# Optimization experiments

Measured on AMD Instinct MI355X. Metric: run time of the kernel, lower is better.

## Reference

```python
import jax, jax.numpy as jnp
import numpy as np

N = 2048          # num nodes
C = 256           # dense_dim per input
EMB = 3 * C       # 768
H = 8             # num_heads
D = EMB // H      # 96 head_dim
ALPHA = 0.2       # leaky relu slope
SCALE = D ** -0.5


def setup_inputs() -> dict:
    key = jax.random.key(0)
    ks = jax.random.split(key, 9)
    sd = EMB ** -0.5
    return {
        "eh": jax.random.normal(ks[0], (N, C), jnp.float32),
        "er": jax.random.normal(ks[1], (N, C), jnp.float32),
        "et": jax.random.normal(ks[2], (N, C), jnp.float32),
        "h_id": jax.random.randint(ks[3], (N,), 0, 32),
        "W_w": jax.random.normal(ks[4], (EMB, EMB), jnp.float32) * sd,
        "a": jax.random.normal(ks[5], (2 * D, 1), jnp.float32) * (2 * D) ** -0.5,
        "proj_w": jax.random.normal(ks[6], (EMB, EMB), jnp.float32) * sd,
        "proj_b": jnp.zeros((EMB,), jnp.float32),
        "skip_w": jax.random.normal(ks[7], (EMB, EMB), jnp.float32) * sd,
        "skip_b": jnp.zeros((EMB,), jnp.float32),
    }


def reference(eh, er, et, h_id, W_w, a, proj_w, proj_b, skip_w, skip_b):
    n = eh.shape[0]
    e = jnp.concatenate([eh, er, et], axis=-1)            # [N, EMB]
    Wh = (e @ W_w.T).reshape(n, H, D)                     # [N, H, D]

    # score = leakyrelu(a1 . Wh_scrambled[i] + a2 . Wh[j]) * scale
    a1, a2 = a[:D, 0], a[D:, 0]
    s1 = Wh @ a1                                          # [N, H]
    s2 = Wh @ a2                                          # [N, H]
    # torch's Wh.repeat(1,1,N).view(N*N,H,D) reads head (j*H + h)//N for pair (i,j,h)
    qidx = (jnp.arange(n)[:, None] * H + jnp.arange(H)[None, :]) // n  # [N, H]
    x = s1[:, qidx] + s2[None, :, :]                      # [N, N, H]
    e_ij = jnp.where(x >= 0, x, ALPHA * x) * SCALE

    mask = h_id[:, None] != h_id[None, :]                 # [N, N]
    e_ij = jnp.where(mask[:, :, None], -jnp.inf, e_ij)
    attn = jax.nn.softmax(e_ij, axis=1)                   # softmax over neighbors j

    out = jnp.einsum('ijh,jhd->ihd', attn, Wh).reshape(n, H * D)
    out = out @ proj_w.T + proj_b                         # [N, EMB]
    skip = e @ skip_w.T + skip_b                          # [N, EMB]
    return skip + out
```

## Files before the change

kernel.cpp:

```cpp
#include <hip/hip_runtime.h>
#include <hip/hip_bf16.h>

#define N_NODES 2048
#define EMB 768
#define NH 8
#define DH 96
#define ALPHA 0.2f
#define SCALE 0.10206207261596575f
#define NGMAX 192

typedef __bf16 bf16x8 __attribute__((ext_vector_type(8)));
typedef float f32x4 __attribute__((ext_vector_type(4)));
typedef __attribute__((address_space(3))) unsigned int lds_u32;
typedef __attribute__((address_space(1))) const unsigned int glb_u32;

union pack4 { ushort4 u; __hip_bfloat16 h[4]; };

__global__ __launch_bounds__(256) void prep_kernel(
    const float* __restrict__ eh, const float* __restrict__ er, const float* __restrict__ et,
    const float* __restrict__ W0, const float* __restrict__ W1, const float* __restrict__ W2,
    __hip_bfloat16* __restrict__ e, __hip_bfloat16* __restrict__ o0,
    __hip_bfloat16* __restrict__ o1, __hip_bfloat16* __restrict__ o2, int* __restrict__ cnt)
{
    const int b = blockIdx.x;
    const int gtid = b * 256 + threadIdx.x;
    if (gtid < 32) cnt[gtid] = 0;
    const float* src;
    __hip_bfloat16* dst;
    if (b < 1536) {
        int idx = gtid * 4;
        int i = idx / EMB, c = idx % EMB;
        if (c < 256)      src = eh + i * 256 + c;
        else if (c < 512) src = er + i * 256 + (c - 256);
        else              src = et + i * 256 + (c - 512);
        dst = e + (size_t)i * EMB + c;
    } else {
        const int WSZ = EMB * EMB;
        int idx = (gtid - 1536 * 256) * 4;
        if (idx < WSZ)          { src = W0 + idx;           dst = o0 + idx; }
        else if (idx < 2 * WSZ) { src = W1 + idx - WSZ;     dst = o1 + idx - WSZ; }
        else                    { src = W2 + idx - 2 * WSZ; dst = o2 + idx - 2 * WSZ; }
    }
    float4 v = *reinterpret_cast<const float4*>(src);
    pack4 p;
    p.h[0] = __float2bfloat16(v.x);
    p.h[1] = __float2bfloat16(v.y);
    p.h[2] = __float2bfloat16(v.z);
    p.h[3] = __float2bfloat16(v.w);
    *reinterpret_cast<ushort4*>(dst) = p.u;
}

__device__ __forceinline__ void stage_tile(
    const __hip_bfloat16* __restrict__ src, int row0, int k0,
    __hip_bfloat16* lds, int wave, int lane)
{
#pragma unroll
    for (int r = 0; r < 2; r++) {
        const int L = wave * 128 + r * 64 + lane;
        const int row = L >> 3;
        const int cb = (L & 7) ^ (row & 7);
        const __hip_bfloat16* g = src + (size_t)(row0 + row) * EMB + k0 + cb * 8;
        __builtin_amdgcn_global_load_lds(
            (glb_u32*)g, (lds_u32*)(lds + (size_t)(wave * 128 + r * 64) * 8), 16, 0, 0);
    }
}

__global__ __launch_bounds__(256) void gemm_nt_kernel(
    const __hip_bfloat16* __restrict__ A1, const __hip_bfloat16* __restrict__ B1, int ns1,
    const __hip_bfloat16* __restrict__ A2, const __hip_bfloat16* __restrict__ B2, int ns2,
    const float* __restrict__ bias1, const float* __restrict__ bias2,
    float* __restrict__ Cf)
{
    __shared__ __attribute__((aligned(16))) __hip_bfloat16 sm[2][2][4096];

    const int t = threadIdx.x;
    const int lane = t & 63, wave = t >> 6;
    const int wm = wave >> 1, wn = wave & 1;
    const int bm = blockIdx.y * 64, bn = blockIdx.x * 64;
    const int l15 = lane & 15, quad = lane >> 4;
    const int NS = ns1 + ns2;

    f32x4 acc00 = {0.f,0.f,0.f,0.f}, acc01 = {0.f,0.f,0.f,0.f};
    f32x4 acc10 = {0.f,0.f,0.f,0.f}, acc11 = {0.f,0.f,0.f,0.f};

    stage_tile(A1, bm, 0, &sm[0][0][0], wave, lane);
    stage_tile(B1, bn, 0, &sm[0][1][0], wave, lane);

    const int rA = wm * 32 + l15;
    const int rB = wn * 32 + l15;
    const int xa = rA & 7, xb = rB & 7;

    for (int s = 0; s < NS; s++) {
        __syncthreads();
        if (s + 1 < NS) {
            const int sn = s + 1;
            const __hip_bfloat16* As = (sn < ns1) ? A1 : A2;
            const __hip_bfloat16* Bs = (sn < ns1) ? B1 : B2;
            const int k0 = ((sn < ns1) ? sn : sn - ns1) * 64;
            stage_tile(As, bm, k0, &sm[sn & 1][0][0], wave, lane);
            stage_tile(Bs, bn, k0, &sm[sn & 1][1][0], wave, lane);
        }
        const __hip_bfloat16* At = &sm[s & 1][0][0];
        const __hip_bfloat16* Bt = &sm[s & 1][1][0];
#pragma unroll
        for (int ks = 0; ks < 2; ks++) {
            const int cq = ks * 4 + quad;
            bf16x8 a0 = *(const bf16x8*)(At + ((size_t)rA        * 8 + (cq ^ xa)) * 8);
            bf16x8 a1 = *(const bf16x8*)(At + ((size_t)(rA + 16) * 8 + (cq ^ xa)) * 8);
            bf16x8 b0 = *(const bf16x8*)(Bt + ((size_t)rB        * 8 + (cq ^ xb)) * 8);
            bf16x8 b1 = *(const bf16x8*)(Bt + ((size_t)(rB + 16) * 8 + (cq ^ xb)) * 8);
            acc00 = __builtin_amdgcn_mfma_f32_16x16x32_bf16(a0, b0, acc00, 0, 0, 0);
            acc01 = __builtin_amdgcn_mfma_f32_16x16x32_bf16(a0, b1, acc01, 0, 0, 0);
            acc10 = __builtin_amdgcn_mfma_f32_16x16x32_bf16(a1, b0, acc10, 0, 0, 0);
            acc11 = __builtin_amdgcn_mfma_f32_16x16x32_bf16(a1, b1, acc11, 0, 0, 0);
        }
    }

    const int col0 = bn + wn * 32 + l15;
    const int col1 = col0 + 16;
    float bv0 = 0.f, bv1 = 0.f;
    if (bias1 != nullptr) {
        bv0 = bias1[col0] + bias2[col0];
        bv1 = bias1[col1] + bias2[col1];
    }
    const int r0 = bm + wm * 32 + quad * 4;
#pragma unroll
    for (int r = 0; r < 4; r++) {
        const int row0 = r0 + r, row1 = r0 + 16 + r;
        Cf[(size_t)row0 * EMB + col0] = acc00[r] + bv0;
        Cf[(size_t)row0 * EMB + col1] = acc01[r] + bv1;
        Cf[(size_t)row1 * EMB + col0] = acc10[r] + bv0;
        Cf[(size_t)row1 * EMB + col1] = acc11[r] + bv1;
    }
}

__global__ __launch_bounds__(256) void s12g_kernel(
    const float* __restrict__ Wh, const float* __restrict__ a,
    float* __restrict__ s1, float* __restrict__ s2,
    const int* __restrict__ h_id, int* __restrict__ cnt, int* __restrict__ lists)
{
    int gid = blockIdx.x * 256 + threadIdx.x;
    if (gid < N_NODES) {
        int g = h_id[gid];
        int p = atomicAdd(&cnt[g], 1);
        lists[g * N_NODES + p] = gid;
    }
    int i = gid >> 3, h = gid & 7;
    const float* wr = Wh + (size_t)i * EMB + h * DH;
    float acc1 = 0.f, acc2 = 0.f;
    for (int d = 0; d < DH; d++) {
        float w = wr[d];
        acc1 += w * a[d];
        acc2 += w * a[DH + d];
    }
    s1[gid] = acc1;
    s2[gid] = acc2;
}

__global__ __launch_bounds__(256) void attn_kernel(
    const float* __restrict__ Wh, const float* __restrict__ s1, const float* __restrict__ s2,
    const int* __restrict__ cnt, const int* __restrict__ lists,
    __hip_bfloat16* __restrict__ out)
{
    const int g  = blockIdx.x & 31;
    const int h  = (blockIdx.x >> 5) & 7;
    const int dh = blockIdx.x >> 8;
    const int t  = threadIdx.x;

    __shared__ int   jb[NGMAX];
    __shared__ int   qg[NGMAX];
    __shared__ float s2g[NGMAX];
    __shared__ float s1g[NGMAX][9];
    __shared__ float Whg[NGMAX][48];

    const int ng = min(cnt[g], NGMAX);
    const int* gl = lists + g * N_NODES;

    for (int j = t; j < ng; j += 256) {
        int node = gl[j];
        jb[j]  = node;
        qg[j]  = node >> 8;
        s2g[j] = s2[node * 8 + h];
        float4 v0 = *reinterpret_cast<const float4*>(s1 + node * 8);
        float4 v1 = *reinterpret_cast<const float4*>(s1 + node * 8 + 4);
        s1g[j][0] = v0.x; s1g[j][1] = v0.y; s1g[j][2] = v0.z; s1g[j][3] = v0.w;
        s1g[j][4] = v1.x; s1g[j][5] = v1.y; s1g[j][6] = v1.z; s1g[j][7] = v1.w;
    }
    __syncthreads();
    for (int idx = t; idx < ng * 12; idx += 256) {
        int jc = idx / 12, dq = idx % 12;
        float4 v = *reinterpret_cast<const float4*>(
            Wh + (size_t)jb[jc] * EMB + h * DH + dh * 48 + dq * 4);
        *reinterpret_cast<float4*>(&Whg[jc][dq * 4]) = v;
    }
    __syncthreads();

    if (t < ng) {
        float m = -1e30f;
        for (int j = 0; j < ng; j++) {
            float x = s1g[t][qg[j]] + s2g[j];
            float ev = (x >= 0.f ? x : ALPHA * x) * SCALE;
            m = fmaxf(m, ev);
        }
        float S = 0.f;
        for (int j = 0; j < ng; j++) {
            float x = s1g[t][qg[j]] + s2g[j];
            float ev = (x >= 0.f ? x : ALPHA * x) * SCALE;
            S += __expf(ev - m);
        }
        const float ri = 1.f / S;

        float acc[48];
#pragma unroll
        for (int d = 0; d < 48; d++) acc[d] = 0.f;
        for (int j = 0; j < ng; j++) {
            float x = s1g[t][qg[j]] + s2g[j];
            float ev = (x >= 0.f ? x : ALPHA * x) * SCALE;
            float p = __expf(ev - m) * ri;
#pragma unroll
            for (int d = 0; d < 48; d++) acc[d] += p * Whg[j][d];
        }
        __hip_bfloat16* po = out + (size_t)jb[t] * EMB + h * DH + dh * 48;
#pragma unroll
        for (int d = 0; d < 48; d += 4) {
            pack4 pk;
            pk.h[0] = __float2bfloat16(acc[d]);
            pk.h[1] = __float2bfloat16(acc[d + 1]);
            pk.h[2] = __float2bfloat16(acc[d + 2]);
            pk.h[3] = __float2bfloat16(acc[d + 3]);
            *reinterpret_cast<ushort4*>(po + d) = pk.u;
        }
    }
}

extern "C" void kernel_launch(void* const* d_in, const int* in_sizes, int n_in,
                              void* d_out, int out_size, void* d_ws, size_t ws_size,
                              hipStream_t stream)
{
    const float* eh     = (const float*)d_in[0];
    const float* er     = (const float*)d_in[1];
    const float* et     = (const float*)d_in[2];
    const int*   h_id   = (const int*)d_in[3];
    const float* W_w    = (const float*)d_in[4];
    const float* a      = (const float*)d_in[5];
    const float* proj_w = (const float*)d_in[6];
    const float* proj_b = (const float*)d_in[7];
    const float* skip_w = (const float*)d_in[8];
    const float* skip_b = (const float*)d_in[9];
    float* out = (float*)d_out;

    char* ws = (char*)d_ws;
    __hip_bfloat16* e_ws   = (__hip_bfloat16*)(ws);
    float*          Wh_ws  = (float*)(ws + 3145728);
    __hip_bfloat16* at_ws  = (__hip_bfloat16*)(ws + 9437184);
    __hip_bfloat16* Wb_ws  = (__hip_bfloat16*)(ws + 12582912);
    __hip_bfloat16* Pb_ws  = (__hip_bfloat16*)(ws + 13762560);
    __hip_bfloat16* Sb_ws  = (__hip_bfloat16*)(ws + 14942208);
    float*          s1_ws  = (float*)(ws + 16121856);
    float*          s2_ws  = (float*)(ws + 16187392);
    int*            cnt_ws = (int*)(ws + 16252928);
    int*            lst_ws = (int*)(ws + 16253056);

    prep_kernel<<<3264, 256, 0, stream>>>(eh, er, et, W_w, proj_w, skip_w,
                                          e_ws, Wb_ws, Pb_ws, Sb_ws, cnt_ws);

    gemm_nt_kernel<<<dim3(12, 32), 256, 0, stream>>>(
        e_ws, Wb_ws, 12, nullptr, nullptr, 0, nullptr, nullptr, Wh_ws);

    s12g_kernel<<<64, 256, 0, stream>>>(Wh_ws, a, s1_ws, s2_ws, h_id, cnt_ws, lst_ws);

    attn_kernel<<<512, 256, 0, stream>>>(Wh_ws, s1_ws, s2_ws, cnt_ws, lst_ws, at_ws);

    gemm_nt_kernel<<<dim3(12, 32), 256, 0, stream>>>(
        at_ws, Pb_ws, 12, e_ws, Sb_ws, 12, proj_b, skip_b, out);
}
```

Measured before the change: 142.3 us.

## Fuse all stages into one persistent kernel with software grid barriers

Replaces the five launches with a zero kernel plus one persistent mega-kernel of 256 blocks that runs conversion, the Wh GEMM, the score dot products, attention and the output GEMM, separated by atomic grid barriers. GEMM tiles grow to a K-step of 128 with a 16-way swizzle and are looped over by the persistent blocks. The attention stage splits the 48-wide head slice across the four waves so all 256 threads work. This removes launch gaps and tail effects, but relies on all 256 blocks being co-resident. The 384 GEMM tiles also land unevenly across 256 blocks.

```diff
diff --git a/kernel.cpp b/kernel.cpp
--- a/kernel.cpp
+++ b/kernel.cpp
@@ -8,6 +8,8 @@
 #define ALPHA 0.2f
 #define SCALE 0.10206207261596575f
 #define NGMAX 192
+#define NB 256
+#define WSZ (EMB * EMB)
 
 typedef __bf16 bf16x8 __attribute__((ext_vector_type(8)));
 typedef float f32x4 __attribute__((ext_vector_type(4)));
@@ -16,221 +18,250 @@
 
 union pack4 { ushort4 u; __hip_bfloat16 h[4]; };
 
-__global__ __launch_bounds__(256) void prep_kernel(
-    const float* __restrict__ eh, const float* __restrict__ er, const float* __restrict__ et,
-    const float* __restrict__ W0, const float* __restrict__ W1, const float* __restrict__ W2,
-    __hip_bfloat16* __restrict__ e, __hip_bfloat16* __restrict__ o0,
-    __hip_bfloat16* __restrict__ o1, __hip_bfloat16* __restrict__ o2, int* __restrict__ cnt)
-{
-    const int b = blockIdx.x;
-    const int gtid = b * 256 + threadIdx.x;
-    if (gtid < 32) cnt[gtid] = 0;
-    const float* src;
-    __hip_bfloat16* dst;
-    if (b < 1536) {
-        int idx = gtid * 4;
-        int i = idx / EMB, c = idx % EMB;
-        if (c < 256)      src = eh + i * 256 + c;
-        else if (c < 512) src = er + i * 256 + (c - 256);
-        else              src = et + i * 256 + (c - 512);
-        dst = e + (size_t)i * EMB + c;
-    } else {
-        const int WSZ = EMB * EMB;
-        int idx = (gtid - 1536 * 256) * 4;
-        if (idx < WSZ)          { src = W0 + idx;           dst = o0 + idx; }
-        else if (idx < 2 * WSZ) { src = W1 + idx - WSZ;     dst = o1 + idx - WSZ; }
-        else                    { src = W2 + idx - 2 * WSZ; dst = o2 + idx - 2 * WSZ; }
-    }
-    float4 v = *reinterpret_cast<const float4*>(src);
-    pack4 p;
-    p.h[0] = __float2bfloat16(v.x);
-    p.h[1] = __float2bfloat16(v.y);
-    p.h[2] = __float2bfloat16(v.z);
-    p.h[3] = __float2bfloat16(v.w);
-    *reinterpret_cast<ushort4*>(dst) = p.u;
-}
-
-__device__ __forceinline__ void stage_tile(
+struct AttnLds {
+    int   jb[NGMAX];
+    int   qg[NGMAX];
+    float s2g[NGMAX];
+    float s1g[NGMAX][9];
+    float Whg[NGMAX][48];
+};
+
+__device__ __forceinline__ void grid_barrier(int* bar, int target)
+{
+    __syncthreads();
+    if (threadIdx.x == 0) {
+        __threadfence();
+        __hip_atomic_fetch_add(bar, 1, __ATOMIC_ACQ_REL, __HIP_MEMORY_SCOPE_AGENT);
+        while (__hip_atomic_load(bar, __ATOMIC_ACQUIRE, __HIP_MEMORY_SCOPE_AGENT) < target)
+            __builtin_amdgcn_s_sleep(1);
+        __threadfence();
+    }
+    __syncthreads();
+}
+
+__device__ __forceinline__ void stage128(
     const __hip_bfloat16* __restrict__ src, int row0, int k0,
     __hip_bfloat16* lds, int wave, int lane)
 {
 #pragma unroll
-    for (int r = 0; r < 2; r++) {
-        const int L = wave * 128 + r * 64 + lane;
-        const int row = L >> 3;
-        const int cb = (L & 7) ^ (row & 7);
+    for (int i = 0; i < 4; i++) {
+        const int c0 = wave * 256 + i * 64;
+        const int c = c0 + lane;
+        const int row = c >> 4;
+        const int cb = (c & 15) ^ (row & 15);
         const __hip_bfloat16* g = src + (size_t)(row0 + row) * EMB + k0 + cb * 8;
-        __builtin_amdgcn_global_load_lds(
-            (glb_u32*)g, (lds_u32*)(lds + (size_t)(wave * 128 + r * 64) * 8), 16, 0, 0);
-    }
-}
-
-__global__ __launch_bounds__(256) void gemm_nt_kernel(
+        __builtin_amdgcn_global_load_lds((glb_u32*)g, (lds_u32*)(lds + c0 * 8), 16, 0, 0);
+    }
+}
+
+__device__ __forceinline__ void gemm_tiles(
     const __hip_bfloat16* __restrict__ A1, const __hip_bfloat16* __restrict__ B1, int ns1,
     const __hip_bfloat16* __restrict__ A2, const __hip_bfloat16* __restrict__ B2, int ns2,
     const float* __restrict__ bias1, const float* __restrict__ bias2,
-    float* __restrict__ Cf)
-{
-    __shared__ __attribute__((aligned(16))) __hip_bfloat16 sm[2][2][4096];
-
+    float* __restrict__ Cf, __hip_bfloat16* sm)
+{
     const int t = threadIdx.x;
     const int lane = t & 63, wave = t >> 6;
     const int wm = wave >> 1, wn = wave & 1;
-    const int bm = blockIdx.y * 64, bn = blockIdx.x * 64;
     const int l15 = lane & 15, quad = lane >> 4;
     const int NS = ns1 + ns2;
-
-    f32x4 acc00 = {0.f,0.f,0.f,0.f}, acc01 = {0.f,0.f,0.f,0.f};
-    f32x4 acc10 = {0.f,0.f,0.f,0.f}, acc11 = {0.f,0.f,0.f,0.f};
-
-    stage_tile(A1, bm, 0, &sm[0][0][0], wave, lane);
-    stage_tile(B1, bn, 0, &sm[0][1][0], wave, lane);
-
-    const int rA = wm * 32 + l15;
-    const int rB = wn * 32 + l15;
-    const int xa = rA & 7, xb = rB & 7;
-
-    for (int s = 0; s < NS; s++) {
+    const int rA = wm * 32 + l15, rB = wn * 32 + l15;
+
+    for (int T = blockIdx.x; T < 384; T += NB) {
+        const int bm = (T & 31) * 64, bn = (T >> 5) * 64;
+        f32x4 acc00 = {0.f,0.f,0.f,0.f}, acc01 = {0.f,0.f,0.f,0.f};
+        f32x4 acc10 = {0.f,0.f,0.f,0.f}, acc11 = {0.f,0.f,0.f,0.f};
+
         __syncthreads();
-        if (s + 1 < NS) {
-            const int sn = s + 1;
-            const __hip_bfloat16* As = (sn < ns1) ? A1 : A2;
-            const __hip_bfloat16* Bs = (sn < ns1) ? B1 : B2;
-            const int k0 = ((sn < ns1) ? sn : sn - ns1) * 64;
-            stage_tile(As, bm, k0, &sm[sn & 1][0][0], wave, lane);
-            stage_tile(Bs, bn, k0, &sm[sn & 1][1][0], wave, lane);
-        }
-        const __hip_bfloat16* At = &sm[s & 1][0][0];
-        const __hip_bfloat16* Bt = &sm[s & 1][1][0];
-#pragma unroll
-        for (int ks = 0; ks < 2; ks++) {
-            const int cq = ks * 4 + quad;
-            bf16x8 a0 = *(const bf16x8*)(At + ((size_t)rA        * 8 + (cq ^ xa)) * 8);
-            bf16x8 a1 = *(const bf16x8*)(At + ((size_t)(rA + 16) * 8 + (cq ^ xa)) * 8);
-            bf16x8 b0 = *(const bf16x8*)(Bt + ((size_t)rB        * 8 + (cq ^ xb)) * 8);
-            bf16x8 b1 = *(const bf16x8*)(Bt + ((size_t)(rB + 16) * 8 + (cq ^ xb)) * 8);
-            acc00 = __builtin_amdgcn_mfma_f32_16x16x32_bf16(a0, b0, acc00, 0, 0, 0);
-            acc01 = __builtin_amdgcn_mfma_f32_16x16x32_bf16(a0, b1, acc01, 0, 0, 0);
-            acc10 = __builtin_amdgcn_mfma_f32_16x16x32_bf16(a1, b0, acc10, 0, 0, 0);
-            acc11 = __builtin_amdgcn_mfma_f32_16x16x32_bf16(a1, b1, acc11, 0, 0, 0);
-        }
-    }
-
-    const int col0 = bn + wn * 32 + l15;
-    const int col1 = col0 + 16;
-    float bv0 = 0.f, bv1 = 0.f;
-    if (bias1 != nullptr) {
-        bv0 = bias1[col0] + bias2[col0];
-        bv1 = bias1[col1] + bias2[col1];
-    }
-    const int r0 = bm + wm * 32 + quad * 4;
-#pragma unroll
-    for (int r = 0; r < 4; r++) {
-        const int row0 = r0 + r, row1 = r0 + 16 + r;
-        Cf[(size_t)row0 * EMB + col0] = acc00[r] + bv0;
-        Cf[(size_t)row0 * EMB + col1] = acc01[r] + bv1;
-        Cf[(size_t)row1 * EMB + col0] = acc10[r] + bv0;
-        Cf[(size_t)row1 * EMB + col1] = acc11[r] + bv1;
-    }
-}
-
-__global__ __launch_bounds__(256) void s12g_kernel(
-    const float* __restrict__ Wh, const float* __restrict__ a,
+        stage128(A1, bm, 0, sm, wave, lane);
+        stage128(B1, bn, 0, sm + 8192, wave, lane);
+
+        for (int s = 0; s < NS; s++) {
+            __syncthreads();
+            if (s + 1 < NS) {
+                const int sn = s + 1;
+                const __hip_bfloat16* As = (sn < ns1) ? A1 : A2;
+                const __hip_bfloat16* Bs = (sn < ns1) ? B1 : B2;
+                const int k0 = ((sn < ns1) ? sn : sn - ns1) * 128;
+                __hip_bfloat16* dst = sm + (sn & 1) * 16384;
+                stage128(As, bm, k0, dst, wave, lane);
+                stage128(Bs, bn, k0, dst + 8192, wave, lane);
+            }
+            const __hip_bfloat16* At = sm + (s & 1) * 16384;
+            const __hip_bfloat16* Bt = At + 8192;
+#pragma unroll
+            for (int ks = 0; ks < 4; ks++) {
+                const int cq = ks * 4 + quad;
+                bf16x8 a0 = *(const bf16x8*)(At + (size_t)(rA * 16        + (cq ^ l15)) * 8);
+                bf16x8 a1 = *(const bf16x8*)(At + (size_t)((rA + 16) * 16 + (cq ^ l15)) * 8);
+                bf16x8 b0 = *(const bf16x8*)(Bt + (size_t)(rB * 16        + (cq ^ l15)) * 8);
+                bf16x8 b1 = *(const bf16x8*)(Bt + (size_t)((rB + 16) * 16 + (cq ^ l15)) * 8);
+                acc00 = __builtin_amdgcn_mfma_f32_16x16x32_bf16(a0, b0, acc00, 0, 0, 0);
+                acc01 = __builtin_amdgcn_mfma_f32_16x16x32_bf16(a0, b1, acc01, 0, 0, 0);
+                acc10 = __builtin_amdgcn_mfma_f32_16x16x32_bf16(a1, b0, acc10, 0, 0, 0);
+                acc11 = __builtin_amdgcn_mfma_f32_16x16x32_bf16(a1, b1, acc11, 0, 0, 0);
+            }
+        }
+
+        const int col0 = bn + wn * 32 + l15;
+        const int col1 = col0 + 16;
+        float bv0 = 0.f, bv1 = 0.f;
+        if (bias1 != nullptr) {
+            bv0 = bias1[col0] + bias2[col0];
+            bv1 = bias1[col1] + bias2[col1];
+        }
+        const int r0 = bm + wm * 32 + quad * 4;
+#pragma unroll
+        for (int r = 0; r < 4; r++) {
+            const int row0 = r0 + r, row1 = r0 + 16 + r;
+            Cf[(size_t)row0 * EMB + col0] = acc00[r] + bv0;
+            Cf[(size_t)row0 * EMB + col1] = acc01[r] + bv1;
+            Cf[(size_t)row1 * EMB + col0] = acc10[r] + bv0;
+            Cf[(size_t)row1 * EMB + col1] = acc11[r] + bv1;
+        }
+    }
+}
+
+__global__ void zero_kernel(int* p)
+{
+    if (threadIdx.x < 64) p[threadIdx.x] = 0;
+}
+
+__global__ __launch_bounds__(256) void mega_kernel(
+    const float* __restrict__ eh, const float* __restrict__ er, const float* __restrict__ et,
+    const int* __restrict__ h_id, const float* __restrict__ W_w, const float* __restrict__ av,
+    const float* __restrict__ proj_w, const float* __restrict__ proj_b,
+    const float* __restrict__ skip_w, const float* __restrict__ skip_b,
+    __hip_bfloat16* __restrict__ e, float* __restrict__ Wh, __hip_bfloat16* __restrict__ at,
+    __hip_bfloat16* __restrict__ Wb, __hip_bfloat16* __restrict__ Pb, __hip_bfloat16* __restrict__ Sb,
     float* __restrict__ s1, float* __restrict__ s2,
-    const int* __restrict__ h_id, int* __restrict__ cnt, int* __restrict__ lists)
-{
-    int gid = blockIdx.x * 256 + threadIdx.x;
-    if (gid < N_NODES) {
-        int g = h_id[gid];
+    int* __restrict__ cnt, int* __restrict__ bar, int* __restrict__ lists,
+    float* __restrict__ out)
+{
+    __shared__ __attribute__((aligned(16))) char smem[65536];
+    const int t = threadIdx.x;
+    const int gtid = blockIdx.x * 256 + t;
+
+    for (int c4 = gtid; c4 < 393216; c4 += NB * 256) {
+        int idx = c4 * 4, i = idx / EMB, c = idx % EMB;
+        const float* src = (c < 256) ? eh + i * 256 + c
+                         : (c < 512) ? er + i * 256 + (c - 256)
+                                     : et + i * 256 + (c - 512);
+        float4 v = *reinterpret_cast<const float4*>(src);
+        pack4 p;
+        p.h[0] = __float2bfloat16(v.x); p.h[1] = __float2bfloat16(v.y);
+        p.h[2] = __float2bfloat16(v.z); p.h[3] = __float2bfloat16(v.w);
+        *reinterpret_cast<ushort4*>(e + (size_t)i * EMB + c) = p.u;
+    }
+    for (int c4 = gtid; c4 < 442368; c4 += NB * 256) {
+        int idx = c4 * 4;
+        const float* src; __hip_bfloat16* dst;
+        if (idx < WSZ)          { src = W_w    + idx;           dst = Wb + idx; }
+        else if (idx < 2 * WSZ) { src = proj_w + idx - WSZ;     dst = Pb + idx - WSZ; }
+        else                    { src = skip_w + idx - 2 * WSZ; dst = Sb + idx - 2 * WSZ; }
+        float4 v = *reinterpret_cast<const float4*>(src);
+        pack4 p;
+        p.h[0] = __float2bfloat16(v.x); p.h[1] = __float2bfloat16(v.y);
+        p.h[2] = __float2bfloat16(v.z); p.h[3] = __float2bfloat16(v.w);
+        *reinterpret_cast<ushort4*>(dst) = p.u;
+    }
+    if (gtid < N_NODES) {
+        int g = h_id[gtid];
         int p = atomicAdd(&cnt[g], 1);
-        lists[g * N_NODES + p] = gid;
-    }
-    int i = gid >> 3, h = gid & 7;
-    const float* wr = Wh + (size_t)i * EMB + h * DH;
-    float acc1 = 0.f, acc2 = 0.f;
-    for (int d = 0; d < DH; d++) {
-        float w = wr[d];
-        acc1 += w * a[d];
-        acc2 += w * a[DH + d];
-    }
-    s1[gid] = acc1;
-    s2[gid] = acc2;
-}
-
-__global__ __launch_bounds__(256) void attn_kernel(
-    const float* __restrict__ Wh, const float* __restrict__ s1, const float* __restrict__ s2,
-    const int* __restrict__ cnt, const int* __restrict__ lists,
-    __hip_bfloat16* __restrict__ out)
-{
-    const int g  = blockIdx.x & 31;
-    const int h  = (blockIdx.x >> 5) & 7;
-    const int dh = blockIdx.x >> 8;
-    const int t  = threadIdx.x;
-
-    __shared__ int   jb[NGMAX];
-    __shared__ int   qg[NGMAX];
-    __shared__ float s2g[NGMAX];
-    __shared__ float s1g[NGMAX][9];
-    __shared__ float Whg[NGMAX][48];
-
-    const int ng = min(cnt[g], NGMAX);
-    const int* gl = lists + g * N_NODES;
-
-    for (int j = t; j < ng; j += 256) {
-        int node = gl[j];
-        jb[j]  = node;
-        qg[j]  = node >> 8;
-        s2g[j] = s2[node * 8 + h];
-        float4 v0 = *reinterpret_cast<const float4*>(s1 + node * 8);
-        float4 v1 = *reinterpret_cast<const float4*>(s1 + node * 8 + 4);
-        s1g[j][0] = v0.x; s1g[j][1] = v0.y; s1g[j][2] = v0.z; s1g[j][3] = v0.w;
-        s1g[j][4] = v1.x; s1g[j][5] = v1.y; s1g[j][6] = v1.z; s1g[j][7] = v1.w;
-    }
-    __syncthreads();
-    for (int idx = t; idx < ng * 12; idx += 256) {
-        int jc = idx / 12, dq = idx % 12;
-        float4 v = *reinterpret_cast<const float4*>(
-            Wh + (size_t)jb[jc] * EMB + h * DH + dh * 48 + dq * 4);
-        *reinterpret_cast<float4*>(&Whg[jc][dq * 4]) = v;
-    }
-    __syncthreads();
-
-    if (t < ng) {
-        float m = -1e30f;
-        for (int j = 0; j < ng; j++) {
-            float x = s1g[t][qg[j]] + s2g[j];
-            float ev = (x >= 0.f ? x : ALPHA * x) * SCALE;
-            m = fmaxf(m, ev);
-        }
-        float S = 0.f;
-        for (int j = 0; j < ng; j++) {
-            float x = s1g[t][qg[j]] + s2g[j];
-            float ev = (x >= 0.f ? x : ALPHA * x) * SCALE;
-            S += __expf(ev - m);
-        }
-        const float ri = 1.f / S;
-
-        float acc[48];
-#pragma unroll
-        for (int d = 0; d < 48; d++) acc[d] = 0.f;
-        for (int j = 0; j < ng; j++) {
-            float x = s1g[t][qg[j]] + s2g[j];
-            float ev = (x >= 0.f ? x : ALPHA * x) * SCALE;
-            float p = __expf(ev - m) * ri;
-#pragma unroll
-            for (int d = 0; d < 48; d++) acc[d] += p * Whg[j][d];
-        }
-        __hip_bfloat16* po = out + (size_t)jb[t] * EMB + h * DH + dh * 48;
-#pragma unroll
-        for (int d = 0; d < 48; d += 4) {
-            pack4 pk;
-            pk.h[0] = __float2bfloat16(acc[d]);
-            pk.h[1] = __float2bfloat16(acc[d + 1]);
-            pk.h[2] = __float2bfloat16(acc[d + 2]);
-            pk.h[3] = __float2bfloat16(acc[d + 3]);
-            *reinterpret_cast<ushort4*>(po + d) = pk.u;
-        }
-    }
+        lists[g * N_NODES + p] = gtid;
+    }
+
+    grid_barrier(bar, NB);
+
+    gemm_tiles(e, Wb, 6, nullptr, nullptr, 0, nullptr, nullptr, Wh, (__hip_bfloat16*)smem);
+
+    grid_barrier(bar, 2 * NB);
+
+    if (gtid < N_NODES * NH) {
+        int i = gtid >> 3, h = gtid & 7;
+        const float* wr = Wh + (size_t)i * EMB + h * DH;
+        float acc1 = 0.f, acc2 = 0.f;
+        for (int d = 0; d < DH; d++) {
+            float w = wr[d];
+            acc1 += w * av[d];
+            acc2 += w * av[DH + d];
+        }
+        s1[gtid] = acc1;
+        s2[gtid] = acc2;
+    }
+
+    grid_barrier(bar, 3 * NB);
+
+    {
+        AttnLds& AL = *reinterpret_cast<AttnLds*>(smem);
+        const int lane = t & 63, wave = t >> 6;
+        for (int v = blockIdx.x; v < 512; v += NB) {
+            __syncthreads();
+            const int g = v & 31, h = (v >> 5) & 7, dh = v >> 8;
+            const int ng = min(cnt[g], NGMAX);
+            const int* gl = lists + g * N_NODES;
+            for (int j = t; j < ng; j += 256) {
+                int node = gl[j];
+                AL.jb[j]  = node;
+                AL.qg[j]  = node >> 8;
+                AL.s2g[j] = s2[node * 8 + h];
+                float4 v0 = *reinterpret_cast<const float4*>(s1 + node * 8);
+                float4 v1 = *reinterpret_cast<const float4*>(s1 + node * 8 + 4);
+                AL.s1g[j][0] = v0.x; AL.s1g[j][1] = v0.y; AL.s1g[j][2] = v0.z; AL.s1g[j][3] = v0.w;
+                AL.s1g[j][4] = v1.x; AL.s1g[j][5] = v1.y; AL.s1g[j][6] = v1.z; AL.s1g[j][7] = v1.w;
+            }
+            __syncthreads();
+            for (int idx = t; idx < ng * 12; idx += 256) {
+                int jc = idx / 12, dq = idx % 12;
+                float4 v4 = *reinterpret_cast<const float4*>(
+                    Wh + (size_t)AL.jb[jc] * EMB + h * DH + dh * 48 + dq * 4);
+                *reinterpret_cast<float4*>(&AL.Whg[jc][dq * 4]) = v4;
+            }
+            __syncthreads();
+            for (int n0 = 0; n0 < ng; n0 += 64) {
+                const int tn = n0 + lane;
+                if (tn < ng) {
+                    float m = -1e30f;
+                    for (int j = 0; j < ng; j++) {
+                        float x = AL.s1g[tn][AL.qg[j]] + AL.s2g[j];
+                        float ev = (x >= 0.f ? x : ALPHA * x) * SCALE;
+                        m = fmaxf(m, ev);
+                    }
+                    float S = 0.f;
+                    for (int j = 0; j < ng; j++) {
+                        float x = AL.s1g[tn][AL.qg[j]] + AL.s2g[j];
+                        float ev = (x >= 0.f ? x : ALPHA * x) * SCALE;
+                        S += __expf(ev - m);
+                    }
+                    const float ri = 1.f / S;
+                    float acc[12];
+#pragma unroll
+                    for (int d = 0; d < 12; d++) acc[d] = 0.f;
+                    for (int j = 0; j < ng; j++) {
+                        float x = AL.s1g[tn][AL.qg[j]] + AL.s2g[j];
+                        float ev = (x >= 0.f ? x : ALPHA * x) * SCALE;
+                        float p = __expf(ev - m) * ri;
+#pragma unroll
+                        for (int d = 0; d < 12; d++) acc[d] += p * AL.Whg[j][wave * 12 + d];
+                    }
+                    __hip_bfloat16* po = at + (size_t)AL.jb[tn] * EMB + h * DH + dh * 48 + wave * 12;
+#pragma unroll
+                    for (int d = 0; d < 12; d += 4) {
+                        pack4 pk;
+                        pk.h[0] = __float2bfloat16(acc[d]);
+                        pk.h[1] = __float2bfloat16(acc[d + 1]);
+                        pk.h[2] = __float2bfloat16(acc[d + 2]);
+                        pk.h[3] = __float2bfloat16(acc[d + 3]);
+                        *reinterpret_cast<ushort4*>(po + d) = pk.u;
+                    }
+                }
+            }
+        }
+    }
+
+    grid_barrier(bar, 4 * NB);
+
+    gemm_tiles(at, Pb, 6, e, Sb, 6, proj_b, skip_b, out, (__hip_bfloat16*)smem);
 }
 
 extern "C" void kernel_launch(void* const* d_in, const int* in_sizes, int n_in,
@@ -259,18 +290,13 @@
     float*          s1_ws  = (float*)(ws + 16121856);
     float*          s2_ws  = (float*)(ws + 16187392);
     int*            cnt_ws = (int*)(ws + 16252928);
-    int*            lst_ws = (int*)(ws + 16253056);
-
-    prep_kernel<<<3264, 256, 0, stream>>>(eh, er, et, W_w, proj_w, skip_w,
-                                          e_ws, Wb_ws, Pb_ws, Sb_ws, cnt_ws);
-
-    gemm_nt_kernel<<<dim3(12, 32), 256, 0, stream>>>(
-        e_ws, Wb_ws, 12, nullptr, nullptr, 0, nullptr, nullptr, Wh_ws);
-
-    s12g_kernel<<<64, 256, 0, stream>>>(Wh_ws, a, s1_ws, s2_ws, h_id, cnt_ws, lst_ws);
-
-    attn_kernel<<<512, 256, 0, stream>>>(Wh_ws, s1_ws, s2_ws, cnt_ws, lst_ws, at_ws);
-
-    gemm_nt_kernel<<<dim3(12, 32), 256, 0, stream>>>(
-        at_ws, Pb_ws, 12, e_ws, Sb_ws, 12, proj_b, skip_b, out);
-}
+    int*            bar_ws = (int*)(ws + 16253056);
+    int*            lst_ws = (int*)(ws + 16253184);
+
+    zero_kernel<<<1, 64, 0, stream>>>(cnt_ws);
+
+    mega_kernel<<<NB, 256, 0, stream>>>(
+        eh, er, et, h_id, W_w, a, proj_w, proj_b, skip_w, skip_b,
+        e_ws, Wh_ws, at_ws, Wb_ws, Pb_ws, Sb_ws, s1_ws, s2_ws,
+        cnt_ws, bar_ws, lst_ws, out);
+}
```

Measured after the change: 336.9 us. 137% more time.

## Fuse attention score projections and group lists into the Wh GEMM epilogue

Applied to the files above, without the earlier changes.

The GEMM tile widens from 64 to 96 columns so each block covers exactly one head. That lets the Wh GEMM epilogue compute the s1/s2 dot products with a shuffle reduction and atomic adds, and the group-list construction also moves into that kernel. This removes the separate s12g kernel launch and its re-read of Wh. In exchange the prep kernel must zero s1/s2 first, the GEMM grid shrinks to fewer, larger blocks, and the float atomics make the summation order nondeterministic.

```diff
diff --git a/kernel.cpp b/kernel.cpp
--- a/kernel.cpp
+++ b/kernel.cpp
@@ -8,6 +8,7 @@
 #define ALPHA 0.2f
 #define SCALE 0.10206207261596575f
 #define NGMAX 192
+#define WSZ (EMB * EMB)
 
 typedef __bf16 bf16x8 __attribute__((ext_vector_type(8)));
 typedef float f32x4 __attribute__((ext_vector_type(4)));
@@ -20,11 +21,19 @@
     const float* __restrict__ eh, const float* __restrict__ er, const float* __restrict__ et,
     const float* __restrict__ W0, const float* __restrict__ W1, const float* __restrict__ W2,
     __hip_bfloat16* __restrict__ e, __hip_bfloat16* __restrict__ o0,
-    __hip_bfloat16* __restrict__ o1, __hip_bfloat16* __restrict__ o2, int* __restrict__ cnt)
+    __hip_bfloat16* __restrict__ o1, __hip_bfloat16* __restrict__ o2,
+    int* __restrict__ cnt, float* __restrict__ s12z)
 {
     const int b = blockIdx.x;
-    const int gtid = b * 256 + threadIdx.x;
-    if (gtid < 32) cnt[gtid] = 0;
+    const int t = threadIdx.x;
+    if (b >= 3264) {
+        int zi = (b - 3264) * 256 + t;
+        float4 z = {0.f, 0.f, 0.f, 0.f};
+        *reinterpret_cast<float4*>(s12z + (size_t)zi * 4) = z;
+        if (zi < 32) cnt[zi] = 0;
+        return;
+    }
+    const int gtid = b * 256 + t;
     const float* src;
     __hip_bfloat16* dst;
     if (b < 1536) {
@@ -35,7 +44,6 @@
         else              src = et + i * 256 + (c - 512);
         dst = e + (size_t)i * EMB + c;
     } else {
-        const int WSZ = EMB * EMB;
         int idx = (gtid - 1536 * 256) * 4;
         if (idx < WSZ)          { src = W0 + idx;           dst = o0 + idx; }
         else if (idx < 2 * WSZ) { src = W1 + idx - WSZ;     dst = o1 + idx - WSZ; }
@@ -50,45 +58,70 @@
     *reinterpret_cast<ushort4*>(dst) = p.u;
 }
 
-__device__ __forceinline__ void stage_tile(
-    const __hip_bfloat16* __restrict__ src, int row0, int k0,
-    __hip_bfloat16* lds, int wave, int lane)
-{
-#pragma unroll
-    for (int r = 0; r < 2; r++) {
-        const int L = wave * 128 + r * 64 + lane;
+__device__ __forceinline__ void stage_ab(
+    const __hip_bfloat16* __restrict__ A, int rowA0,
+    const __hip_bfloat16* __restrict__ B, int rowB0, int k0,
+    __hip_bfloat16* smA, __hip_bfloat16* smB, int wave, int lane)
+{
+#pragma unroll
+    for (int i = 0; i < 2; i++) {
+        const int c0 = wave * 128 + i * 64;
+        const int L = c0 + lane;
         const int row = L >> 3;
         const int cb = (L & 7) ^ (row & 7);
-        const __hip_bfloat16* g = src + (size_t)(row0 + row) * EMB + k0 + cb * 8;
         __builtin_amdgcn_global_load_lds(
-            (glb_u32*)g, (lds_u32*)(lds + (size_t)(wave * 128 + r * 64) * 8), 16, 0, 0);
-    }
-}
-
-__global__ __launch_bounds__(256) void gemm_nt_kernel(
+            (glb_u32*)(A + (size_t)(rowA0 + row) * EMB + k0 + cb * 8),
+            (lds_u32*)(smA + c0 * 8), 16, 0, 0);
+    }
+#pragma unroll
+    for (int i = 0; i < 3; i++) {
+        const int c0 = wave * 192 + i * 64;
+        const int L = c0 + lane;
+        const int row = L >> 3;
+        const int cb = (L & 7) ^ (row & 7);
+        __builtin_amdgcn_global_load_lds(
+            (glb_u32*)(B + (size_t)(rowB0 + row) * EMB + k0 + cb * 8),
+            (lds_u32*)(smB + c0 * 8), 16, 0, 0);
+    }
+}
+
+__global__ __launch_bounds__(256) void gemm_kernel(
     const __hip_bfloat16* __restrict__ A1, const __hip_bfloat16* __restrict__ B1, int ns1,
     const __hip_bfloat16* __restrict__ A2, const __hip_bfloat16* __restrict__ B2, int ns2,
     const float* __restrict__ bias1, const float* __restrict__ bias2,
-    float* __restrict__ Cf)
-{
-    __shared__ __attribute__((aligned(16))) __hip_bfloat16 sm[2][2][4096];
+    float* __restrict__ Cf,
+    const float* __restrict__ av, float* __restrict__ s1, float* __restrict__ s2,
+    const int* __restrict__ h_id, int* __restrict__ cnt, int* __restrict__ lists)
+{
+    __shared__ __attribute__((aligned(16))) __hip_bfloat16 smA[2][4096];
+    __shared__ __attribute__((aligned(16))) __hip_bfloat16 smB[2][6144];
 
     const int t = threadIdx.x;
     const int lane = t & 63, wave = t >> 6;
     const int wm = wave >> 1, wn = wave & 1;
-    const int bm = blockIdx.y * 64, bn = blockIdx.x * 64;
+    const int bm = blockIdx.y * 64, bn = blockIdx.x * 96;
     const int l15 = lane & 15, quad = lane >> 4;
     const int NS = ns1 + ns2;
 
-    f32x4 acc00 = {0.f,0.f,0.f,0.f}, acc01 = {0.f,0.f,0.f,0.f};
-    f32x4 acc10 = {0.f,0.f,0.f,0.f}, acc11 = {0.f,0.f,0.f,0.f};
-
-    stage_tile(A1, bm, 0, &sm[0][0][0], wave, lane);
-    stage_tile(B1, bn, 0, &sm[0][1][0], wave, lane);
+    if (h_id != nullptr) {
+        int fid = (blockIdx.y * 8 + blockIdx.x) * 256 + t;
+        if (fid < N_NODES) {
+            int g = h_id[fid];
+            int p = atomicAdd(&cnt[g], 1);
+            lists[g * N_NODES + p] = fid;
+        }
+    }
+
+    f32x4 acc[2][3];
+#pragma unroll
+    for (int fr = 0; fr < 2; fr++)
+#pragma unroll
+        for (int fc = 0; fc < 3; fc++) acc[fr][fc] = (f32x4){0.f, 0.f, 0.f, 0.f};
+
+    stage_ab(A1, bm, B1, bn, 0, smA[0], smB[0], wave, lane);
 
     const int rA = wm * 32 + l15;
-    const int rB = wn * 32 + l15;
-    const int xa = rA & 7, xb = rB & 7;
+    const int rB = wn * 48 + l15;
 
     for (int s = 0; s < NS; s++) {
         __syncthreads();
@@ -97,64 +130,72 @@
             const __hip_bfloat16* As = (sn < ns1) ? A1 : A2;
             const __hip_bfloat16* Bs = (sn < ns1) ? B1 : B2;
             const int k0 = ((sn < ns1) ? sn : sn - ns1) * 64;
-            stage_tile(As, bm, k0, &sm[sn & 1][0][0], wave, lane);
-            stage_tile(Bs, bn, k0, &sm[sn & 1][1][0], wave, lane);
-        }
-        const __hip_bfloat16* At = &sm[s & 1][0][0];
-        const __hip_bfloat16* Bt = &sm[s & 1][1][0];
+            stage_ab(As, bm, Bs, bn, k0, smA[sn & 1], smB[sn & 1], wave, lane);
+        }
+        const __hip_bfloat16* At = smA[s & 1];
+        const __hip_bfloat16* Bt = smB[s & 1];
 #pragma unroll
         for (int ks = 0; ks < 2; ks++) {
             const int cq = ks * 4 + quad;
-            bf16x8 a0 = *(const bf16x8*)(At + ((size_t)rA        * 8 + (cq ^ xa)) * 8);
-            bf16x8 a1 = *(const bf16x8*)(At + ((size_t)(rA + 16) * 8 + (cq ^ xa)) * 8);
-            bf16x8 b0 = *(const bf16x8*)(Bt + ((size_t)rB        * 8 + (cq ^ xb)) * 8);
-            bf16x8 b1 = *(const bf16x8*)(Bt + ((size_t)(rB + 16) * 8 + (cq ^ xb)) * 8);
-            acc00 = __builtin_amdgcn_mfma_f32_16x16x32_bf16(a0, b0, acc00, 0, 0, 0);
-            acc01 = __builtin_amdgcn_mfma_f32_16x16x32_bf16(a0, b1, acc01, 0, 0, 0);
-            acc10 = __builtin_amdgcn_mfma_f32_16x16x32_bf16(a1, b0, acc10, 0, 0, 0);
-            acc11 = __builtin_amdgcn_mfma_f32_16x16x32_bf16(a1, b1, acc11, 0, 0, 0);
-        }
-    }
-
-    const int col0 = bn + wn * 32 + l15;
-    const int col1 = col0 + 16;
-    float bv0 = 0.f, bv1 = 0.f;
-    if (bias1 != nullptr) {
-        bv0 = bias1[col0] + bias2[col0];
-        bv1 = bias1[col1] + bias2[col1];
-    }
-    const int r0 = bm + wm * 32 + quad * 4;
-#pragma unroll
-    for (int r = 0; r < 4; r++) {
-        const int row0 = r0 + r, row1 = r0 + 16 + r;
-        Cf[(size_t)row0 * EMB + col0] = acc00[r] + bv0;
-        Cf[(size_t)row0 * EMB + col1] = acc01[r] + bv1;
-        Cf[(size_t)row1 * EMB + col0] = acc10[r] + bv0;
-        Cf[(size_t)row1 * EMB + col1] = acc11[r] + bv1;
-    }
-}
-
-__global__ __launch_bounds__(256) void s12g_kernel(
-    const float* __restrict__ Wh, const float* __restrict__ a,
-    float* __restrict__ s1, float* __restrict__ s2,
-    const int* __restrict__ h_id, int* __restrict__ cnt, int* __restrict__ lists)
-{
-    int gid = blockIdx.x * 256 + threadIdx.x;
-    if (gid < N_NODES) {
-        int g = h_id[gid];
-        int p = atomicAdd(&cnt[g], 1);
-        lists[g * N_NODES + p] = gid;
-    }
-    int i = gid >> 3, h = gid & 7;
-    const float* wr = Wh + (size_t)i * EMB + h * DH;
-    float acc1 = 0.f, acc2 = 0.f;
-    for (int d = 0; d < DH; d++) {
-        float w = wr[d];
-        acc1 += w * a[d];
-        acc2 += w * a[DH + d];
-    }
-    s1[gid] = acc1;
-    s2[gid] = acc2;
+            bf16x8 a0 = *(const bf16x8*)(At + (size_t)(rA        * 8 + (cq ^ (rA & 7)))        * 8);
+            bf16x8 a1 = *(const bf16x8*)(At + (size_t)((rA + 16) * 8 + (cq ^ ((rA + 16) & 7))) * 8);
+            bf16x8 b0 = *(const bf16x8*)(Bt + (size_t)(rB        * 8 + (cq ^ (rB & 7)))        * 8);
+            bf16x8 b1 = *(const bf16x8*)(Bt + (size_t)((rB + 16) * 8 + (cq ^ ((rB + 16) & 7))) * 8);
+            bf16x8 b2 = *(const bf16x8*)(Bt + (size_t)((rB + 32) * 8 + (cq ^ ((rB + 32) & 7))) * 8);
+            acc[0][0] = __builtin_amdgcn_mfma_f32_16x16x32_bf16(a0, b0, acc[0][0], 0, 0, 0);
+            acc[0][1] = __builtin_amdgcn_mfma_f32_16x16x32_bf16(a0, b1, acc[0][1], 0, 0, 0);
+            acc[0][2] = __builtin_amdgcn_mfma_f32_16x16x32_bf16(a0, b2, acc[0][2], 0, 0, 0);
+            acc[1][0] = __builtin_amdgcn_mfma_f32_16x16x32_bf16(a1, b0, acc[1][0], 0, 0, 0);
+            acc[1][1] = __builtin_amdgcn_mfma_f32_16x16x32_bf16(a1, b1, acc[1][1], 0, 0, 0);
+            acc[1][2] = __builtin_amdgcn_mfma_f32_16x16x32_bf16(a1, b2, acc[1][2], 0, 0, 0);
+        }
+    }
+
+    float bv[3] = {0.f, 0.f, 0.f};
+    int col[3];
+#pragma unroll
+    for (int fc = 0; fc < 3; fc++) {
+        col[fc] = bn + wn * 48 + fc * 16 + l15;
+        if (bias1 != nullptr) bv[fc] = bias1[col[fc]] + bias2[col[fc]];
+    }
+#pragma unroll
+    for (int fr = 0; fr < 2; fr++) {
+        const int r0 = bm + wm * 32 + fr * 16 + quad * 4;
+#pragma unroll
+        for (int r = 0; r < 4; r++)
+#pragma unroll
+            for (int fc = 0; fc < 3; fc++)
+                Cf[(size_t)(r0 + r) * EMB + col[fc]] = acc[fr][fc][r] + bv[fc];
+    }
+
+    if (av != nullptr) {
+        const int h = blockIdx.x;
+        float a1v[3], a2v[3];
+#pragma unroll
+        for (int fc = 0; fc < 3; fc++) {
+            const int cl = wn * 48 + fc * 16 + l15;
+            a1v[fc] = av[cl];
+            a2v[fc] = av[96 + cl];
+        }
+#pragma unroll
+        for (int fr = 0; fr < 2; fr++) {
+            const int r0 = bm + wm * 32 + fr * 16 + quad * 4;
+#pragma unroll
+            for (int r = 0; r < 4; r++) {
+                float p1 = acc[fr][0][r] * a1v[0] + acc[fr][1][r] * a1v[1] + acc[fr][2][r] * a1v[2];
+                float p2 = acc[fr][0][r] * a2v[0] + acc[fr][1][r] * a2v[1] + acc[fr][2][r] * a2v[2];
+#pragma unroll
+                for (int o = 1; o < 16; o <<= 1) {
+                    p1 += __shfl_xor(p1, o);
+                    p2 += __shfl_xor(p2, o);
+                }
+                if (l15 == 0) {
+                    atomicAdd(&s1[(r0 + r) * 8 + h], p1);
+                    atomicAdd(&s2[(r0 + r) * 8 + h], p2);
+                }
+            }
+        }
+    }
 }
 
 __global__ __launch_bounds__(256) void attn_kernel(
@@ -261,16 +302,16 @@
     int*            cnt_ws = (int*)(ws + 16252928);
     int*            lst_ws = (int*)(ws + 16253056);
 
-    prep_kernel<<<3264, 256, 0, stream>>>(eh, er, et, W_w, proj_w, skip_w,
-                                          e_ws, Wb_ws, Pb_ws, Sb_ws, cnt_ws);
-
-    gemm_nt_kernel<<<dim3(12, 32), 256, 0, stream>>>(
-        e_ws, Wb_ws, 12, nullptr, nullptr, 0, nullptr, nullptr, Wh_ws);
-
-    s12g_kernel<<<64, 256, 0, stream>>>(Wh_ws, a, s1_ws, s2_ws, h_id, cnt_ws, lst_ws);
+    prep_kernel<<<3296, 256, 0, stream>>>(eh, er, et, W_w, proj_w, skip_w,
+                                          e_ws, Wb_ws, Pb_ws, Sb_ws, cnt_ws, s1_ws);
+
+    gemm_kernel<<<dim3(8, 32), 256, 0, stream>>>(
+        e_ws, Wb_ws, 12, nullptr, nullptr, 0, nullptr, nullptr, Wh_ws,
+        a, s1_ws, s2_ws, h_id, cnt_ws, lst_ws);
 
     attn_kernel<<<512, 256, 0, stream>>>(Wh_ws, s1_ws, s2_ws, cnt_ws, lst_ws, at_ws);
 
-    gemm_nt_kernel<<<dim3(12, 32), 256, 0, stream>>>(
-        at_ws, Pb_ws, 12, e_ws, Sb_ws, 12, proj_b, skip_b, out);
-}
+    gemm_kernel<<<dim3(8, 32), 256, 0, stream>>>(
+        at_ws, Pb_ws, 12, e_ws, Sb_ws, 12, proj_b, skip_b, out,
+        nullptr, nullptr, nullptr, nullptr, nullptr, nullptr);
+}
```

New measurement: 147.9 us. +3.9%, slower.
